# Kernel optimization log

Measured on AMD Instinct MI355X. Metric: run time of the kernel, lower is better.

The kernel has to match this reference:

```python
import jax, jax.numpy as jnp
import numpy as np

B, T, N, CIN, C, L, NC, S = 8, 64, 200, 200, 128, 2, 2, 100
SPARSITY = 30


def bn(x, g, b, eps=1e-5):
    # BatchNorm1d forward with batch statistics (training-mode math, biased var)
    m = x.mean(0)
    v = x.var(0)
    return (x - m) / jnp.sqrt(v + eps) * g + b


def ln(x, g, b, eps=1e-5):
    m = x.mean(-1, keepdims=True)
    v = x.var(-1, keepdims=True)
    return (x - m) / jnp.sqrt(v + eps) * g + b


def setup_inputs() -> dict:
    key = jax.random.key(0)
    ks = iter(jax.random.split(key, 64))

    def nrm(shape, s=0.02):
        return jax.random.normal(next(ks), shape, jnp.float32) * s

    return dict(
        fMRI_v=jax.random.normal(next(ks), (B, T, N, CIN), jnp.float32),
        fMRI_a=jax.random.uniform(next(ks), (B, T, N, N), jnp.float32),
        sMRI_trad=jax.random.normal(next(ks), (B, S), jnp.float32),
        sMRI_deep=jnp.zeros((B, 1, 8, 8, 8), jnp.float32),
        csatt=1, CA_MOD=0,
        w_init=nrm((CIN, C)), b_init=jnp.zeros((C,), jnp.float32),
        gin_eps=jnp.zeros((L,), jnp.float32),
        gin_w1=nrm((L, C, C)), gin_b1=jnp.zeros((L, C), jnp.float32),
        gin_bn1_g=jnp.ones((L, C), jnp.float32), gin_bn1_b=jnp.zeros((L, C), jnp.float32),
        gin_w2=nrm((L, C, C)), gin_b2=jnp.zeros((L, C), jnp.float32),
        gin_bn2_g=jnp.ones((L, C), jnp.float32), gin_bn2_b=jnp.zeros((L, C), jnp.float32),
        sero_w=nrm((L, C, C)), sero_b=jnp.zeros((L, C), jnp.float32),
        sero_bn_g=jnp.ones((L, C), jnp.float32), sero_bn_b=jnp.zeros((L, C), jnp.float32),
        sero_aw=nrm((L, C, N)), sero_ab=jnp.zeros((L, N), jnp.float32),
        tr_wqkv=nrm((L, C, 3 * C)), tr_bqkv=jnp.zeros((L, 3 * C), jnp.float32),
        tr_wo=nrm((L, C, C)), tr_bo=jnp.zeros((L, C), jnp.float32),
        tr_ln1_g=jnp.ones((L, C), jnp.float32), tr_ln1_b=jnp.zeros((L, C), jnp.float32),
        tr_ln2_g=jnp.ones((L, C), jnp.float32), tr_ln2_b=jnp.zeros((L, C), jnp.float32),
        tr_w1=nrm((L, C, 2 * C)), tr_b1=jnp.zeros((L, 2 * C), jnp.float32),
        tr_w2=nrm((L, 2 * C, C)), tr_b2=jnp.zeros((L, C), jnp.float32),
        cls_w=nrm((L, C, NC)), cls_b=jnp.zeros((L, NC), jnp.float32),
        smri_w=nrm((S, C)), smri_b=jnp.zeros((C,), jnp.float32),
        smri_bn_g=jnp.ones((C,), jnp.float32), smri_bn_b=jnp.zeros((C,), jnp.float32),
    )


def reference(fMRI_v, fMRI_a, sMRI_trad, sMRI_deep, csatt, CA_MOD,
              w_init, b_init, gin_eps,
              gin_w1, gin_b1, gin_bn1_g, gin_bn1_b,
              gin_w2, gin_b2, gin_bn2_g, gin_bn2_b,
              sero_w, sero_b, sero_bn_g, sero_bn_b, sero_aw, sero_ab,
              tr_wqkv, tr_bqkv, tr_wo, tr_bo,
              tr_ln1_g, tr_ln1_b, tr_ln2_g, tr_ln2_b,
              tr_w1, tr_b1, tr_w2, tr_b2,
              cls_w, cls_b, smri_w, smri_b, smri_bn_g, smri_bn_b):
    b, t, n = fMRI_a.shape[:3]
    # initial linear over flattened (b t n) tokens
    h3 = (fMRI_v.reshape(-1, fMRI_v.shape[-1]) @ w_init + b_init).reshape(b, t, n, -1)
    # _collate_adjacency: per-(sample,timepoint) percentile threshold -> block-diag sparse
    # with all-ones values; equivalent to a batched masked matmul.
    thr = jnp.percentile(fMRI_a, 100 - SPARSITY, axis=(-2, -1), keepdims=True)
    mask = (fMRI_a > thr).astype(h3.dtype)  # [b,t,n,n]

    logit = jnp.zeros((b, cls_w.shape[-1]), h3.dtype)
    latents, node_attns, time_attns = [], [], []
    scale = 1.0 / jnp.sqrt(jnp.asarray(h3.shape[-1], h3.dtype))
    for l in range(L):
        # LayerGIN: note the original feeds h3 (initial features) to EVERY layer
        agg = jnp.einsum('btij,btjc->btic', mask, h3) + gin_eps[l] * h3
        x = agg.reshape(-1, agg.shape[-1])
        x = jax.nn.relu(bn(x @ gin_w1[l] + gin_b1[l], gin_bn1_g[l], gin_bn1_b[l]))
        x = jax.nn.relu(bn(x @ gin_w2[l] + gin_b2[l], gin_bn2_g[l], gin_bn2_b[l]))
        hb = x.reshape(b, t, n, -1).transpose(1, 0, 2, 3)  # (t,b,n,c)
        # ModuleSERO readout (node_axis=2)
        xr = hb.mean(2)  # (t,b,c)
        e = jax.nn.gelu(bn(xr.reshape(t * b, -1) @ sero_w[l] + sero_b[l],
                           sero_bn_g[l], sero_bn_b[l]), approximate=False)
        ga = jax.nn.sigmoid(e @ sero_aw[l] + sero_ab[l]).reshape(t, b, n)
        hr = (hb * ga[..., None]).mean(2)  # (t,b,c)
        node_attns.append(ga.transpose(1, 0, 2))  # (b,t,n)
        # ModuleTransformer (single head, post-LN, no residual before ln1)
        qkv = hr @ tr_wqkv[l] + tr_bqkv[l]
        q, k, v = jnp.split(qkv, 3, axis=-1)
        A = jax.nn.softmax(jnp.einsum('tbc,sbc->bts', q, k) * scale, axis=-1)  # (b,t,t)
        att = jnp.einsum('bts,sbc->tbc', A, v) @ tr_wo[l] + tr_bo[l]
        x1 = ln(att, tr_ln1_g[l], tr_ln1_b[l])
        m = jax.nn.relu(x1 @ tr_w1[l] + tr_b1[l]) @ tr_w2[l] + tr_b2[l]
        x2 = ln(x1 + m, tr_ln2_g[l], tr_ln2_b[l])
        time_attns.append(A)
        lat = x2.sum(0)  # cls_token='sum' over time
        logit = logit + lat @ cls_w[l] + cls_b[l]
        latents.append(lat)
    feat_fMRI = jnp.stack(latents, 1).mean(1)  # (b,c)
    feat_sMRI = bn(sMRI_trad @ smri_w + smri_b, smri_bn_g, smri_bn_b)
    node_attn = jnp.stack(node_attns, 1)  # (b,L,t,n)
    time_attn = jnp.stack(time_attns, 1)  # (b,L,t,t)
    return (logit, feat_fMRI, feat_sMRI, node_attn, time_attn)
```

## Files before the change

### kernel.cpp

```cpp
#include <hip/hip_runtime.h>
#include <math.h>

#define B_   8
#define T_   64
#define N_   200
#define CIN_ 200
#define C_   128
#define L_   2
#define NC_  2
#define S_   100
#define BT_  512
#define RB_  102400

typedef __attribute__((ext_vector_type(8))) short short8v;
typedef __attribute__((ext_vector_type(4))) float f32x4v;

union U4S8 { uint4 u; short8v s; };

__device__ __forceinline__ unsigned short f2bf(float f) {
    unsigned u = __float_as_uint(f);
    unsigned r = (u + 0x7FFFu + ((u >> 16) & 1u)) >> 16;
    return (unsigned short)r;
}
__device__ __forceinline__ float bf2f(unsigned short u) {
// ... 85 lines not shown
        __syncthreads();
    }
    int c_lo_tot = red[0];
    if (tid < 256) part[tid] = hist[4*tid] + hist[4*tid+1] + hist[4*tid+2] + hist[4*tid+3];
    __syncthreads();
    if (tid < 32) {
        int s = 0;
        for (int i = 0; i < 8; i++) s += part[8*tid + i];
        grp[tid] = s;
    }
    __syncthreads();
    if (tid == 0) {
        int r = 27999 - c_lo_tot;
        int cum = 0, g = 0;
        while (cum + grp[g] <= r) cum += grp[g++];
        int t = g * 8;
        while (cum + part[t] <= r) cum += part[t++];
        int b = t * 4;
        while (cum + hist[b] <= r) cum += hist[b++];
        meta[2] = b; meta[3] = cum;
        int r1 = r + 1;
        cum = 0; g = 0;
        while (cum + grp[g] <= r1) cum += grp[g++];
        t = g * 8;
        while (cum + part[t] <= r1) cum += part[t++];
        b = t * 4;
        while (cum + hist[b] <= r1) cum += hist[b++];
        meta[4] = b; meta[5] = r;
    }
    __syncthreads();
    int blo = meta[2], base = meta[3], bhi = meta[4], r = meta[5];
    int m = meta[0]; if (m > 6144) m = 6144;
    for (int i = tid; i < m; i += 1024) {
        float v = candV[i];
        int bin = (int)((v - 0.65f) * 10240.0f);
        bin = bin < 0 ? 0 : (bin > 1023 ? 1023 : bin);
        if (bin >= blo && bin <= bhi) {
            int p = atomicAdd(&meta[1], 1);
            if (p < 256) cand2[p] = v;
        }
    }
    __syncthreads();
    if (tid == 0) {
        int m2 = meta[1]; if (m2 > 256) m2 = 256;
        for (int i = 1; i < m2; i++) {
            float key = cand2[i]; int j = i - 1;
            while (j >= 0 && cand2[j] > key) { cand2[j+1] = cand2[j]; j--; }
            cand2[j+1] = key;
        }
        float s1 = cand2[r - base], s2 = cand2[r + 1 - base];
        float tv = s1 * 0.701171875f + s2 * 0.298828125f;
        thr[bt] = tv;
        s_thr = tv;
    }
    __syncthreads();
    float tv = s_thr;
    for (int i = tid; i < m; i += 1024) {
        if (candV[i] > tv) {
            int vi = candP[i];
            int row = vi / 200, col = vi - row * 200;
            atomicOr(&smask[row * 7 + (col >> 5)], 1u << (col & 31));
        }
    }
    __syncthreads();
    for (int i = tid; i < 1400; i += 1024)
        msk[(long)bt * 1400 + i] = smask[i];
}

__global__ void wtcvt5_kernel(const float* __restrict__ w_init,
                              const float* __restrict__ gin_w1,
                              const float* __restrict__ gin_w2,
                              unsigned short* __restrict__ WT0,
                              unsigned short* __restrict__ WT1,
                              unsigned short* __restrict__ WT2) {
    int grp = blockIdx.x >> 7, c = blockIdx.x & 127;
    const float* w; unsigned short* wt; int K, Kpad;
    if (grp == 0)      { w = w_init;                     wt = WT0;                     K = 200; Kpad = 224; }
    else if (grp <= 2) { w = gin_w1 + (grp - 1) * C_ * C_; wt = WT1 + (grp - 1) * 128 * 128; K = 128; Kpad = 128; }
    else               { w = gin_w2 + (grp - 3) * C_ * C_; wt = WT2 + (grp - 3) * 128 * 128; K = 128; Kpad = 128; }
    for (int k = threadIdx.x; k < Kpad; k += 64)
        wt[(long)c * Kpad + k] = f2bf((k < K) ? w[(long)k * 128 + c] : 0.f);
}

template<bool A_BF16, bool BN_IN, bool BIAS_OUT, bool STATS_OUT>
__global__ __launch_bounds__(256) void gemm_direct_kernel(
        const void* __restrict__ xv, int K, int Kstride, int Ksteps,
        const unsigned short* __restrict__ wt, int Kpad,
        const float* __restrict__ bias, const float* __restrict__ statsIn,
        const float* __restrict__ bng, const float* __restrict__ bnb,
        unsigned short* __restrict__ y, float* __restrict__ statsOut) {
    constexpr int ASZ  = A_BF16 ? 8192 : 16384;
    constexpr int BOFF = 2 * ASZ;
    constexpr int NEED = 2 * ASZ + 2 * 8192;
    constexpr int POOL = NEED > 32768 ? NEED : 32768;
    __shared__ unsigned char pool[POOL];
    __shared__ float bnS[128], bnB[128];
    int tid = threadIdx.x;
    if (BN_IN) {
        if (tid < 128) {
            float mm = statsIn[tid] * (1.f / (float)RB_);
            float var = fmaxf(statsIn[128 + tid] * (1.f / (float)RB_) - mm * mm, 0.f);
            float sc = bng[tid] / sqrtf(var + 1e-5f);
            bnS[tid] = sc; bnB[tid] = bnb[tid] - mm * sc;
        }
    }
    int wave = tid >> 6, lane = tid & 63, quad = lane >> 4, m16 = lane & 15;
    long row0g = (long)blockIdx.x * 128;

    auto STAGE = [&](int buf, int ks) {
        #pragma unroll
        for (int j = 0; j < 2; j++) {
            int r = j * 64 + (tid >> 2);
            int c = (tid & 3) ^ ((r >> 1) & 3);
            const char* src = (const char*)wt + (long)r * (Kpad * 2) + ks * 64 + c * 16;
            char* dst = (char*)pool + BOFF + buf * 8192 + j * 4096 + wave * 1024;
            GLL(src, dst);
        }
        if (A_BF16) {
            const char* xb = (const char*)xv;
            #pragma unroll
            for (int j = 0; j < 2; j++) {
                int r = j * 64 + (tid >> 2);
                int c = (tid & 3) ^ ((r >> 1) & 3);
                const char* src = xb + ((row0g + r) * Kstride + ks * 32) * 2 + c * 16;
                char* dst = (char*)pool + buf * ASZ + j * 4096 + wave * 1024;
                GLL(src, dst);
            }
        } else {
            const char* xb = (const char*)xv;
            #pragma unroll
            for (int j = 0; j < 4; j++) {
                int r = j * 32 + (tid >> 3);
                int c = (tid & 7) ^ (r & 7);
                const char* src = xb + ((row0g + r) * Kstride + ks * 32) * 4 + c * 16;
                char* dst = (char*)pool + buf * ASZ + j * 4096 + wave * 1024;
                GLL(src, dst);
            }
        }
    };

    f32x4v acc[2][8];
    #pragma unroll
    for (int i = 0; i < 2; i++)
        #pragma unroll
        for (int j = 0; j < 8; j++) acc[i][j] = (f32x4v){0.f, 0.f, 0.f, 0.f};

    STAGE(0, 0);
    __syncthreads();

    for (int ks = 0; ks < Ksteps; ks++) {
        if (ks + 1 < Ksteps) {
            STAGE((ks + 1) & 1, ks + 1);
            if (A_BF16) asm volatile("s_waitcnt vmcnt(4)" ::: "memory");
            else        asm volatile("s_waitcnt vmcnt(6)" ::: "memory");
        } else {
            asm volatile("s_waitcnt vmcnt(0)" ::: "memory");
        }
        __builtin_amdgcn_s_barrier();
        asm volatile("" ::: "memory");

        const char* Ab = (const char*)pool + (ks & 1) * ASZ;
        const char* Bb = (const char*)pool + BOFF + (ks & 1) * 8192;
        int kf = ks * 32 + quad * 8;
        U4S8 bU[8];
        #pragma unroll
        for (int nt = 0; nt < 8; nt++) {
            int r = nt * 16 + m16;
            int ch = quad ^ ((r >> 1) & 3);
            bU[nt].u = *(const uint4*)(Bb + r * 64 + ch * 16);
        }
        U4S8 aU[2];
        if (A_BF16) {
            #pragma unroll
            for (int mt = 0; mt < 2; mt++) {
                int r = wave * 32 + mt * 16 + m16;
                int ch = quad ^ ((r >> 1) & 3);
                aU[mt].u = *(const uint4*)(Ab + r * 64 + ch * 16);
            }
            if (BN_IN) {
                float4 s0 = *(const float4*)&bnS[kf], s1 = *(const float4*)&bnS[kf + 4];
                float4 b0 = *(const float4*)&bnB[kf], b1 = *(const float4*)&bnB[kf + 4];
                #pragma unroll
                for (int mt = 0; mt < 2; mt++) {
                    uint4 u = aU[mt].u;
                    float f0 = fmaxf(bflo(u.x) * s0.x + b0.x, 0.f);
                    float f1 = fmaxf(bfhi(u.x) * s0.y + b0.y, 0.f);
                    float f2 = fmaxf(bflo(u.y) * s0.z + b0.z, 0.f);
                    float f3 = fmaxf(bfhi(u.y) * s0.w + b0.w, 0.f);
                    float f4 = fmaxf(bflo(u.z) * s1.x + b1.x, 0.f);
                    float f5 = fmaxf(bfhi(u.z) * s1.y + b1.y, 0.f);
                    float f6 = fmaxf(bflo(u.w) * s1.z + b1.z, 0.f);
                    float f7 = fmaxf(bfhi(u.w) * s1.w + b1.w, 0.f);
                    u.x = packbf(f0, f1); u.y = packbf(f2, f3);
                    u.z = packbf(f4, f5); u.w = packbf(f6, f7);
                    aU[mt].u = u;
                }
            }
        } else {
            #pragma unroll
            for (int mt = 0; mt < 2; mt++) {
                int r = wave * 32 + mt * 16 + m16;
                int swz = r & 7;
                const char* base = Ab + r * 128;
                float4 v0 = *(const float4*)(base + ((2 * quad) ^ swz) * 16);
                float4 v1 = *(const float4*)(base + ((2 * quad + 1) ^ swz) * 16);
                uint4 o;
                o.x = packbf(v0.x, v0.y); o.y = packbf(v0.z, v0.w);
                o.z = packbf(v1.x, v1.y); o.w = packbf(v1.z, v1.w);
                aU[mt].u = o;
            }
        }
        #pragma unroll
        for (int nt = 0; nt < 8; nt++) {
            acc[0][nt] = __builtin_amdgcn_mfma_f32_16x16x32_bf16(aU[0].s, bU[nt].s, acc[0][nt], 0, 0, 0);
            acc[1][nt] = __builtin_amdgcn_mfma_f32_16x16x32_bf16(aU[1].s, bU[nt].s, acc[1][nt], 0, 0, 0);
        }
        asm volatile("s_waitcnt lgkmcnt(0)" ::: "memory");
        __builtin_amdgcn_s_barrier();
        asm volatile("" ::: "memory");
    }
    if (!A_BF16 && (K & 31) != 0) {
        int kf = Ksteps * 32 + quad * 8;
        U4S8 bU[8];
        #pragma unroll
        for (int nt = 0; nt < 8; nt++)
            bU[nt].u = *(const uint4*)&wt[(long)(nt * 16 + m16) * Kpad + kf];
        U4S8 aU[2];
        const float* x = (const float*)xv;
        #pragma unroll
        for (int mt = 0; mt < 2; mt++) {
            uint4 o = {0u, 0u, 0u, 0u};
            if (kf + 8 <= K) {
                const float* p = &x[(row0g + wave * 32 + mt * 16 + m16) * Kstride + kf];
                float4 v0 = *(const float4*)p;
                float4 v1 = *(const float4*)(p + 4);
                o.x = packbf(v0.x, v0.y); o.y = packbf(v0.z, v0.w);
                o.z = packbf(v1.x, v1.y); o.w = packbf(v1.z, v1.w);
            }
            aU[mt].u = o;
        }
        #pragma unroll
        for (int nt = 0; nt < 8; nt++) {
            acc[0][nt] = __builtin_amdgcn_mfma_f32_16x16x32_bf16(aU[0].s, bU[nt].s, acc[0][nt], 0, 0, 0);
            acc[1][nt] = __builtin_amdgcn_mfma_f32_16x16x32_bf16(aU[1].s, bU[nt].s, acc[1][nt], 0, 0, 0);
        }
    }

    unsigned short* trans = (unsigned short*)pool;
    float sAcc[8], qAcc[8];
    #pragma unroll
    for (int nt = 0; nt < 8; nt++) {
        int col = nt * 16 + m16;
        float bv = BIAS_OUT ? bias[col] : 0.f;
        float s = 0.f, q = 0.f;
        #pragma unroll
        for (int mt = 0; mt < 2; mt++) {
            int lrb = wave * 32 + mt * 16 + quad * 4;
            #pragma unroll
            for (int i = 0; i < 4; i++) {
                int lr = lrb + i;
                float v = acc[mt][nt][i] + bv;
                trans[lr * 128 + (col ^ ((lr & 6) << 2))] = f2bf(v);
                if (STATS_OUT) { s += v; q += v * v; }
            }
        }
        sAcc[nt] = s; qAcc[nt] = q;
    }
    __syncthreads();
    #pragma unroll
    for (int rnd = 0; rnd < 8; rnd++) {
        int row = rnd * 16 + (tid >> 4), ch = tid & 15;
        uint4 v = *(const uint4*)&trans[row * 128 + ((ch * 8) ^ ((row & 6) << 2))];
        *(uint4*)&y[(row0g + row) * 128 + ch * 8] = v;
    }
    if (STATS_OUT) {
        __syncthreads();
        float* redS = (float*)pool;
        float* redQ = redS + 2048;
        #pragma unroll
        for (int nt = 0; nt < 8; nt++) {
            int col = nt * 16 + m16;
            redS[col * 16 + wave * 4 + quad] = sAcc[nt];
            redQ[col * 16 + wave * 4 + quad] = qAcc[nt];
        }
        __syncthreads();
        if (tid < 128) {
            float s = 0.f, q = 0.f;
            #pragma unroll
            for (int j = 0; j < 16; j++) { s += redS[tid * 16 + j]; q += redQ[tid * 16 + j]; }
            atomicAdd(&statsOut[tid], s);
            atomicAdd(&statsOut[128 + tid], q);
        }
    }
}

__global__ __launch_bounds__(256) void h3gemmT_kernel(
        const float* __restrict__ xv, const unsigned short* __restrict__ wt,
        const float* __restrict__ bias,
        unsigned short* __restrict__ yrow, unsigned short* __restrict__ zt) {
    __shared__ unsigned char pool[49152];
    int tid = threadIdx.x;
    int wave = tid >> 6, lane = tid & 63, quad = lane >> 4, m16 = lane & 15;
    long row0g = (long)blockIdx.x * 128;

    auto STAGE = [&](int buf, int ks) {
        #pragma unroll
        for (int j = 0; j < 2; j++) {
            int r = j * 64 + (tid >> 2);
            int c = (tid & 3) ^ ((r >> 1) & 3);
            const char* src = (const char*)wt + (long)r * 448 + ks * 64 + c * 16;
            char* dst = (char*)pool + 32768 + buf * 8192 + j * 4096 + wave * 1024;
            GLL(src, dst);
        }
        const char* xb = (const char*)xv;
        #pragma unroll
        for (int j = 0; j < 4; j++) {
            int r = j * 32 + (tid >> 3);
            int c = (tid & 7) ^ (r & 7);
            const char* src = xb + ((row0g + r) * 200 + ks * 32) * 4 + c * 16;
            char* dst = (char*)pool + buf * 16384 + j * 4096 + wave * 1024;
            GLL(src, dst);
        }
    };

    f32x4v acc[2][8];
    #pragma unroll
    for (int i = 0; i < 2; i++)
        #pragma unroll
        for (int j = 0; j < 8; j++) acc[i][j] = (f32x4v){0.f, 0.f, 0.f, 0.f};

    STAGE(0, 0);
    __syncthreads();

    for (int ks = 0; ks < 6; ks++) {
        if (ks + 1 < 6) {
            STAGE((ks + 1) & 1, ks + 1);
            asm volatile("s_waitcnt vmcnt(6)" ::: "memory");
        } else {
            asm volatile("s_waitcnt vmcnt(0)" ::: "memory");
        }
        __builtin_amdgcn_s_barrier();
        asm volatile("" ::: "memory");

        const char* Ab = (const char*)pool + (ks & 1) * 16384;
        const char* Bb = (const char*)pool + 32768 + (ks & 1) * 8192;
        U4S8 bU[8];
        #pragma unroll
        for (int nt = 0; nt < 8; nt++) {
            int r = nt * 16 + m16;
            int ch = quad ^ ((r >> 1) & 3);
            bU[nt].u = *(const uint4*)(Bb + r * 64 + ch * 16);
        }
        U4S8 aU[2];
        #pragma unroll
        for (int mt = 0; mt < 2; mt++) {
            int r = wave * 32 + mt * 16 + m16;
            int swz = r & 7;
            const char* base = Ab + r * 128;
            float4 v0 = *(const float4*)(base + ((2 * quad) ^ swz) * 16);
            float4 v1 = *(const float4*)(base + ((2 * quad + 1) ^ swz) * 16);
            uint4 o;
            o.x = packbf(v0.x, v0.y); o.y = packbf(v0.z, v0.w);
            o.z = packbf(v1.x, v1.y); o.w = packbf(v1.z, v1.w);
            aU[mt].u = o;
        }
        #pragma unroll
        for (int nt = 0; nt < 8; nt++) {
            acc[0][nt] = __builtin_amdgcn_mfma_f32_16x16x32_bf16(aU[0].s, bU[nt].s, acc[0][nt], 0, 0, 0);
            acc[1][nt] = __builtin_amdgcn_mfma_f32_16x16x32_bf16(aU[1].s, bU[nt].s, acc[1][nt], 0, 0, 0);
        }
        asm volatile("s_waitcnt lgkmcnt(0)" ::: "memory");
        __builtin_amdgcn_s_barrier();
        asm volatile("" ::: "memory");
    }
    {
        int kf = 192 + quad * 8;
        U4S8 bU[8];
        #pragma unroll
        for (int nt = 0; nt < 8; nt++)
            bU[nt].u = *(const uint4*)&wt[(long)(nt * 16 + m16) * 224 + kf];
        U4S8 aU[2];
        #pragma unroll
        for (int mt = 0; mt < 2; mt++) {
            uint4 o = {0u, 0u, 0u, 0u};
            if (kf + 8 <= 200) {
                const float* p = &xv[(row0g + wave * 32 + mt * 16 + m16) * 200 + kf];
                float4 v0 = *(const float4*)p;
                float4 v1 = *(const float4*)(p + 4);
                o.x = packbf(v0.x, v0.y); o.y = packbf(v0.z, v0.w);
                o.z = packbf(v1.x, v1.y); o.w = packbf(v1.z, v1.w);
            }
            aU[mt].u = o;
        }
        #pragma unroll
        for (int nt = 0; nt < 8; nt++) {
            acc[0][nt] = __builtin_amdgcn_mfma_f32_16x16x32_bf16(aU[0].s, bU[nt].s, acc[0][nt], 0, 0, 0);
            acc[1][nt] = __builtin_amdgcn_mfma_f32_16x16x32_bf16(aU[1].s, bU[nt].s, acc[1][nt], 0, 0, 0);
        }
    }

    unsigned short* tile = (unsigned short*)pool;
    #pragma unroll
    for (int nt = 0; nt < 8; nt++) {
        int col = nt * 16 + m16;
        float bv = bias[col];
        #pragma unroll
        for (int mt = 0; mt < 2; mt++) {
            int lrb = wave * 32 + mt * 16 + quad * 4;
            #pragma unroll
            for (int i = 0; i < 4; i++) {
                int lr = lrb + i;
                tile[lr * 128 + (col ^ ((lr & 14) << 2))] = f2bf(acc[mt][nt][i] + bv);
            }
        }
    }
    __syncthreads();
    #pragma unroll
    for (int rnd = 0; rnd < 8; rnd++) {
        int row = rnd * 16 + (tid >> 4), ch = tid & 15;
        uint4 v = *(const uint4*)&tile[row * 128 + ((ch * 8) ^ ((row & 14) << 2))];
        *(uint4*)&yrow[(row0g + row) * 128 + ch * 8] = v;
    }
    int r0 = blockIdx.x * 128;
    int bt0 = r0 / 200, n0 = r0 - bt0 * 200;
    int len0 = 200 - n0; if (len0 > 128) len0 = 128;
    int c = tid & 127, h = tid >> 7;
    #pragma unroll
    for (int u = 0; u < 8; u++) {
        int rl = h * 64 + u * 8;
        unsigned short e[8];
        #pragma unroll
        for (int j = 0; j < 8; j++)
            e[j] = tile[(rl + j) * 128 + (c ^ (((rl + j) & 14) << 2))];
        uint4 o;
        o.x = (unsigned)e[0] | ((unsigned)e[1] << 16);
        o.y = (unsigned)e[2] | ((unsigned)e[3] << 16);
        o.z = (unsigned)e[4] | ((unsigned)e[5] << 16);
        o.w = (unsigned)e[6] | ((unsigned)e[7] << 16);
        int bt, n;
        if (rl < len0) { bt = bt0; n = n0 + rl; } else { bt = bt0 + 1; n = rl - len0; }
        *(uint4*)&zt[((long)bt * 128 + c) * 224 + n] = o;
    }
    if (n0 >= 72) {
        uint4 z = {0u, 0u, 0u, 0u};
        for (int idx = tid; idx < 384; idx += 256) {
            int c2 = idx & 127, u2 = idx >> 7;
            *(uint4*)&zt[((long)bt0 * 128 + c2) * 224 + 200 + u2 * 8] = z;
        }
    }
}

__global__ __launch_bounds__(256) void maskfused_kernel(
        const unsigned* __restrict__ msk, const unsigned short* __restrict__ zt,
        const unsigned short* __restrict__ h3, const unsigned short* __restrict__ w1t,
        const float* __restrict__ geps, int l, const float* __restrict__ b1,
        unsigned short* __restrict__ y, float* __restrict__ statsOut) {
    __shared__ union {
        unsigned short stage[4][4096];
        unsigned short trans[16384];
        struct { float S[2048]; float Q[2048]; } red;
    } u;
    __shared__ unsigned sbits[128 * 7];
    int tid = threadIdx.x;
    int bt = blockIdx.x & 511, half = blockIdx.x >> 9;
    int row0 = half * 128;
    int wave = tid >> 6, lane = tid & 63, quad = lane >> 4, m16 = lane & 15;
    const char* ztb = (const char*)(zt + (long)bt * 128 * 224);

    int sr = tid >> 2, sq = tid & 3;
    auto STAGE = [&](int buf, int kc) {
        #pragma unroll
        for (int j = 0; j < 2; j++) {
            int r = j * 64 + sr;
            int q = sq ^ ((r >> 1) & 3);
            const char* src = ztb + r * 448 + kc * 64 + q * 16;
            char* dst = (char*)&u.stage[buf][0] + j * 4096 + wave * 1024;
            GLL(src, dst);
        }
    };

    STAGE(0, 0); STAGE(1, 1); STAGE(2, 2);
    for (int idx = tid; idx < 896; idx += 256) {
        int gr = row0 + idx / 7;
        sbits[idx] = (gr < N_) ? msk[(long)bt * 1400 + gr * 7 + (idx % 7)] : 0u;
    }
    unsigned ONEu = 0x3F80u;

    f32x4v acc[2][8];
    #pragma unroll
    for (int i = 0; i < 2; i++)
        #pragma unroll
        for (int j = 0; j < 8; j++) acc[i][j] = (f32x4v){0.f, 0.f, 0.f, 0.f};

    __syncthreads();

    for (int kc = 0; kc < 7; kc++) {
        if (kc < 4) STAGE((kc + 3) & 3, kc + 3);
        if (kc == 3)      asm volatile("s_waitcnt vmcnt(6)" ::: "memory");
        else if (kc == 4) asm volatile("s_waitcnt vmcnt(4)" ::: "memory");
        else if (kc == 5) asm volatile("s_waitcnt vmcnt(2)" ::: "memory");
        else if (kc == 6) asm volatile("s_waitcnt vmcnt(0)" ::: "memory");
        __builtin_amdgcn_s_barrier();
        asm volatile("" ::: "memory");

        const char* sb = (const char*)&u.stage[kc & 3][0];
        U4S8 bU[8];
        #pragma unroll
        for (int nt = 0; nt < 8; nt++) {
            int r = nt * 16 + m16;
            int q = quad ^ ((r >> 1) & 3);
            bU[nt].u = *(const uint4*)(sb + r * 64 + q * 16);
        }
        U4S8 aU[2];
        #pragma unroll
        for (int mt = 0; mt < 2; mt++) {
            int lr = wave * 32 + mt * 16 + m16;
            unsigned bits = (sbits[lr * 7 + kc] >> (quad * 8)) & 0xFFu;
            unsigned o[4];
            #pragma unroll
            for (int p = 0; p < 4; p++) {
                unsigned lo = ((bits >> (2 * p)) & 1u) ? ONEu : 0u;
                unsigned hi = ((bits >> (2 * p + 1)) & 1u) ? ONEu : 0u;
                o[p] = lo | (hi << 16);
            }
            aU[mt].u = make_uint4(o[0], o[1], o[2], o[3]);
        }
        #pragma unroll
        for (int nt = 0; nt < 8; nt++) {
            acc[0][nt] = __builtin_amdgcn_mfma_f32_16x16x32_bf16(aU[0].s, bU[nt].s, acc[0][nt], 0, 0, 0);
            acc[1][nt] = __builtin_amdgcn_mfma_f32_16x16x32_bf16(aU[1].s, bU[nt].s, acc[1][nt], 0, 0, 0);
        }
        asm volatile("s_waitcnt lgkmcnt(0)" ::: "memory");
        __builtin_amdgcn_s_barrier();
        asm volatile("" ::: "memory");
    }

    #pragma unroll
    for (int nt = 0; nt < 8; nt++) {
        int col = nt * 16 + m16;
        #pragma unroll
        for (int mt = 0; mt < 2; mt++) {
            int lrb = wave * 32 + mt * 16 + quad * 4;
            #pragma unroll
            for (int i = 0; i < 4; i++) {
                int lr = lrb + i;
                u.trans[lr * 128 + (col ^ ((lr & 6) << 2))] = f2bf(acc[mt][nt][i]);
            }
        }
    }
    __syncthreads();

    float eps = geps[l];
    f32x4v acc2[2][8];
    #pragma unroll
    for (int i = 0; i < 2; i++)
        #pragma unroll
        for (int j = 0; j < 8; j++) acc2[i][j] = (f32x4v){0.f, 0.f, 0.f, 0.f};

    for (int ks = 0; ks < 4; ks++) {
        int kf = ks * 32 + quad * 8;
        U4S8 bU[8];
        #pragma unroll
        for (int nt = 0; nt < 8; nt++)
            bU[nt].u = *(const uint4*)&w1t[(long)(nt * 16 + m16) * 128 + kf];
        U4S8 aU[2];
        #pragma unroll
        for (int mt = 0; mt < 2; mt++) {
            int r = wave * 32 + mt * 16 + m16;
            uint4 mu = *(const uint4*)&u.trans[r * 128 + (kf ^ ((r & 6) << 2))];
            int gr = row0 + r;
            uint4 hu = {0u, 0u, 0u, 0u};
            if (gr < N_) hu = *(const uint4*)&h3[((long)bt * N_ + gr) * 128 + kf];
            float f0 = bflo(mu.x) + eps * bflo(hu.x);
            float f1 = bfhi(mu.x) + eps * bfhi(hu.x);
            float f2 = bflo(mu.y) + eps * bflo(hu.y);
            float f3 = bfhi(mu.y) + eps * bfhi(hu.y);
            float f4 = bflo(mu.z) + eps * bflo(hu.z);
            float f5 = bfhi(mu.z) + eps * bfhi(hu.z);
            float f6 = bflo(mu.w) + eps * bflo(hu.w);
            float f7 = bfhi(mu.w) + eps * bfhi(hu.w);
            uint4 o;
            o.x = packbf(f0, f1); o.y = packbf(f2, f3);
            o.z = packbf(f4, f5); o.w = packbf(f6, f7);
            aU[mt].u = o;
        }
        #pragma unroll
        for (int nt = 0; nt < 8; nt++) {
            acc2[0][nt] = __builtin_amdgcn_mfma_f32_16x16x32_bf16(aU[0].s, bU[nt].s, acc2[0][nt], 0, 0, 0);
            acc2[1][nt] = __builtin_amdgcn_mfma_f32_16x16x32_bf16(aU[1].s, bU[nt].s, acc2[1][nt], 0, 0, 0);
        }
    }
    __syncthreads();

    float sAcc[8], qAcc[8];
    #pragma unroll
    for (int nt = 0; nt < 8; nt++) {
        int col = nt * 16 + m16;
        float bv = b1[col];
        float s = 0.f, q = 0.f;
        #pragma unroll
        for (int mt = 0; mt < 2; mt++) {
            int lrb = wave * 32 + mt * 16 + quad * 4;
            #pragma unroll
            for (int i = 0; i < 4; i++) {
                int lr = lrb + i;
                float v = acc2[mt][nt][i] + bv;
                u.trans[lr * 128 + (col ^ ((lr & 6) << 2))] = f2bf(v);
                if (row0 + lr < N_) { s += v; q += v * v; }
            }
        }
        sAcc[nt] = s; qAcc[nt] = q;
    }
    __syncthreads();
    #pragma unroll
    for (int rnd = 0; rnd < 8; rnd++) {
        int row = rnd * 16 + (tid >> 4), ch = tid & 15;
        int gr = row0 + row;
        uint4 v = *(const uint4*)&u.trans[row * 128 + ((ch * 8) ^ ((row & 6) << 2))];
        if (gr < N_)
            *(uint4*)&y[((long)bt * N_ + gr) * 128 + ch * 8] = v;
    }
    __syncthreads();
    #pragma unroll
    for (int nt = 0; nt < 8; nt++) {
        int col = nt * 16 + m16;
        u.red.S[col * 16 + wave * 4 + quad] = sAcc[nt];
        u.red.Q[col * 16 + wave * 4 + quad] = qAcc[nt];
    }
    __syncthreads();
    if (tid < 128) {
        float s = 0.f, q = 0.f;
        #pragma unroll
        for (int j = 0; j < 16; j++) { s += u.red.S[tid * 16 + j]; q += u.red.Q[tid * 16 + j]; }
        atomicAdd(&statsOut[tid], s);
        atomicAdd(&statsOut[128 + tid], q);
    }
}

__global__ __launch_bounds__(256) void xrE_kernel(
        const unsigned short* __restrict__ raw, const float* __restrict__ stats,
        const float* __restrict__ g, const float* __restrict__ b,
        const float* __restrict__ sw, const float* __restrict__ sb,
        float* __restrict__ E, float* __restrict__ statE) {
    __shared__ float red[256];
    __shared__ float xrrow[128];
    int tid = threadIdx.x, c = tid & 127, hf = tid >> 7;
    int t = blockIdx.x / B_, bb = blockIdx.x % B_;
    const unsigned short* base = raw + ((long)bb * T_ + t) * N_ * C_;
    float m = stats[c] * (1.f / (float)RB_);
    float var = fmaxf(stats[128 + c] * (1.f / (float)RB_) - m * m, 0.f);
    float sc = g[c] / sqrtf(var + 1e-5f);
    float sh = b[c] - m * sc;
    float s = 0.f;
    for (int n = hf * 100; n < hf * 100 + 100; n++)
        s += fmaxf(fmaf(bf2f(base[n * C_ + c]), sc, sh), 0.f);
    red[tid] = s;
    __syncthreads();
    if (hf == 0) xrrow[c] = (red[c] + red[c + 128]) * (1.f / 200.f);
    __syncthreads();
    float acc = 0.f;
    for (int k = hf * 64; k < hf * 64 + 64; k++)
        acc = fmaf(xrrow[k], sw[k * C_ + c], acc);
    red[tid] = acc;
    __syncthreads();
    if (hf == 0) {
        float v = red[c] + red[c + 128] + sb[c];
        E[(long)blockIdx.x * C_ + c] = v;
        atomicAdd(&statE[c], v);
        atomicAdd(&statE[C_ + c], v * v);
    }
}

__global__ __launch_bounds__(256) void ga_kernel(const float* __restrict__ eRaw,
                          const float* __restrict__ stats,
                          const float* __restrict__ sg, const float* __restrict__ sb,
                          const float* __restrict__ aw, const float* __restrict__ ab,
                          float* __restrict__ ga, float* __restrict__ node_out, int l) {
    __shared__ float sx[4 * C_];
    __shared__ float bnS[C_], bnB[C_];
    int tid = threadIdx.x;
    if (tid < C_) {
        float m = stats[tid] * (1.f / (float)BT_);
        float var = fmaxf(stats[C_ + tid] * (1.f / (float)BT_) - m * m, 0.f);
        float inv = 1.f / sqrtf(var + 1e-5f);
        float sc = inv * sg[tid];
        bnS[tid] = sc;
        bnB[tid] = sb[tid] - m * sc;
    }
    __syncthreads();
    long r0 = (long)blockIdx.x * 4;
    for (int idx = tid; idx < 4 * C_; idx += 256) {
        int col = idx & (C_ - 1);
        float v = eRaw[r0 * C_ + idx] * bnS[col] + bnB[col];
        sx[idx] = 0.5f * v * (1.f + erff(v * 0.70710678118654752f));
    }
    __syncthreads();
    int c = tid;
    if (c < N_) {
        float acc[4] = {0.f, 0.f, 0.f, 0.f};
        for (int k = 0; k < C_; k++) {
            float wv = aw[k * N_ + c];
            #pragma unroll
            for (int i = 0; i < 4; i++) acc[i] = fmaf(sx[i * C_ + k], wv, acc[i]);
        }
        float bv = ab[c];
        for (int i = 0; i < 4; i++) {
            int tb = (int)r0 + i;
            int t = tb / B_, b = tb % B_;
            float v = 1.f / (1.f + expf(-(acc[i] + bv)));
            ga[(long)tb * N_ + c] = v;
            node_out[(((long)b * L_ + l) * T_ + t) * N_ + c] = v;
        }
    }
}

__global__ __launch_bounds__(256) void hrQKV_kernel(
// ... 165 lines not shown
    float inv = 1.f / sqrtf(var + 1e-5f);
    for (int b = 0; b < B_; b++) out[b * C_ + c] = (y[b] - m) * inv * g[c] + bb[c];
}

extern "C" void kernel_launch(void* const* d_in, const int* in_sizes, int n_in,
                              void* d_out, int out_size, void* d_ws, size_t ws_size,
                              hipStream_t stream) {
    const float* fv       = (const float*)d_in[0];
    const float* fa       = (const float*)d_in[1];
    const float* trad     = (const float*)d_in[2];
    const float* w_init   = (const float*)d_in[6];
    const float* b_init   = (const float*)d_in[7];
    const float* gin_eps  = (const float*)d_in[8];
    const float* gin_w1   = (const float*)d_in[9];
    const float* gin_b1   = (const float*)d_in[10];
    const float* gbn1g    = (const float*)d_in[11];
    const float* gbn1b    = (const float*)d_in[12];
    const float* gin_w2   = (const float*)d_in[13];
    const float* gin_b2   = (const float*)d_in[14];
    const float* gbn2g    = (const float*)d_in[15];
    const float* gbn2b    = (const float*)d_in[16];
    const float* sero_w   = (const float*)d_in[17];
    const float* sero_b   = (const float*)d_in[18];
    const float* sbng     = (const float*)d_in[19];
    const float* sbnb     = (const float*)d_in[20];
    const float* sero_aw  = (const float*)d_in[21];
    const float* sero_ab  = (const float*)d_in[22];
    const float* wqkv     = (const float*)d_in[23];
    const float* bqkv     = (const float*)d_in[24];
    const float* wo       = (const float*)d_in[25];
    const float* bo       = (const float*)d_in[26];
    const float* ln1g     = (const float*)d_in[27];
    const float* ln1b     = (const float*)d_in[28];
    const float* ln2g     = (const float*)d_in[29];
    const float* ln2b     = (const float*)d_in[30];
    const float* tw1      = (const float*)d_in[31];
    const float* tb1      = (const float*)d_in[32];
    const float* tw2      = (const float*)d_in[33];
    const float* tb2      = (const float*)d_in[34];
    const float* cls_w    = (const float*)d_in[35];
    const float* cls_b    = (const float*)d_in[36];
    const float* smri_w   = (const float*)d_in[37];
    const float* smri_b   = (const float*)d_in[38];
    const float* smri_g   = (const float*)d_in[39];
    const float* smri_bb  = (const float*)d_in[40];

    float* out = (float*)d_out;

    const long SZ_BIG = (long)RB_ * C_;
    unsigned short* H3b = (unsigned short*)d_ws;
    unsigned short* Y1b = H3b + SZ_BIG;
    unsigned short* Y2b = Y1b + SZ_BIG;
    unsigned short* ZTb = Y2b + SZ_BIG;
    float* fbase = (float*)(ZTb + (long)BT_ * 128 * 224);
    float* THR  = fbase;
    float* SBUF = THR + 512;
    float* LAT  = SBUF + 1536;
    float* E    = LAT + 2048;
    float* GA   = E + BT_ * C_;
    float* QKV  = GA + BT_ * N_;
    float* X1   = QKV + BT_ * 3 * C_;
    unsigned short* WT0 = (unsigned short*)(X1 + BT_ * C_);
    unsigned short* WT1 = WT0 + 128 * 224;
    unsigned short* WT2 = WT1 + 2 * 128 * 128;
    unsigned* MSK = (unsigned*)(WT2 + 2 * 128 * 128);

    float* OUT_LOGIT = out;
    float* OUT_FEATS = out + 1040;
    float* OUT_NODE  = out + 2064;
    float* OUT_TIME  = out + 206864;

    wtcvt5_kernel<<<640, 64, 0, stream>>>(w_init, gin_w1, gin_w2, WT0, WT1, WT2);
    hipMemsetAsync(SBUF, 0, (1536 + 2048) * sizeof(float), stream);

    h3gemmT_kernel<<<RB_ / 128, 256, 0, stream>>>(fv, WT0, b_init, H3b, ZTb);
    thr_kernel<<<BT_, 1024, 0, stream>>>(fa, THR, MSK);

    for (int l = 0; l < L_; l++) {
        float* SA = SBUF + l * 768;
        float* SB = SA + 256;
        float* SE = SA + 512;
        maskfused_kernel<<<BT_ * 2, 256, 0, stream>>>(MSK, ZTb, H3b, WT1 + l * 128 * 128,
            gin_eps, l, gin_b1 + l * C_, Y2b, SA);
        gemm_direct_kernel<true, true, true, true><<<RB_ / 128, 256, 0, stream>>>(
            Y2b, 128, 128, 4, WT2 + l * 128 * 128, 128, gin_b2 + l * C_, SA,
            gbn1g + l * C_, gbn1b + l * C_, Y1b, SB);
        xrE_kernel<<<BT_, 256, 0, stream>>>(Y1b, SB, gbn2g + l * C_, gbn2b + l * C_,
            sero_w + l * C_ * C_, sero_b + l * C_, E, SE);
        ga_kernel<<<BT_ / 4, 256, 0, stream>>>(E, SE, sbng + l * C_, sbnb + l * C_,
            sero_aw + l * C_ * N_, sero_ab + l * N_, GA, OUT_NODE, l);
        hrQKV_kernel<<<BT_, 256, 0, stream>>>(Y1b, SB, gbn2g + l * C_, gbn2b + l * C_,
            GA, wqkv + l * C_ * 3 * C_, bqkv + l * 3 * C_, QKV);
        attnln_kernel<<<BT_, 128, 0, stream>>>(QKV, wo + l * C_ * C_, bo + l * C_,
            ln1g + l * C_, ln1b + l * C_, OUT_TIME, X1, l);
        ffn_kernel<<<BT_ / 2, 256, 0, stream>>>(X1, tw1 + l * C_ * 2 * C_, tb1 + l * 2 * C_,
            tw2 + l * 2 * C_ * C_, tb2 + l * C_, ln2g + l * C_, ln2b + l * C_,
            LAT + l * B_ * C_);
    }

    final_kernel<<<5, 256, 0, stream>>>(LAT, cls_w, cls_b, OUT_LOGIT);
    smri_kernel<<<1, 128, 0, stream>>>(trad, smri_w, smri_b, smri_g, smri_bb, OUT_FEATS);
}
```

Baseline: 713.4 us.

## Preload full K tiles into 64KB LDS, replacing double-buffered staging in GEMM kernels

The templated gemm_direct kernel becomes a specialized bngemm kernel that issues all four K-step loads for A and B into a 64KB LDS pool up front. One barrier follows, then the K loop runs with no per-step waits or barriers. maskfused_kernel likewise loads all seven K-chunks at once instead of using a 4-deep rotating stage, and keeps separate LDS regions for the aggregate and transpose buffers so one barrier can be dropped. This removes per-iteration vmcnt waits and barriers, but 64KB+ of LDS per block cuts occupancy to about one or two blocks per CU, which reduces latency hiding across blocks.

```diff
diff --git a/kernel.cpp b/kernel.cpp
--- a/kernel.cpp
+++ b/kernel.cpp
@@ -191,85 +191,55 @@
         wt[(long)c * Kpad + k] = f2bf((k < K) ? w[(long)k * 128 + c] : 0.f);
 }
 
-template<bool A_BF16, bool BN_IN, bool BIAS_OUT, bool STATS_OUT>
-__global__ __launch_bounds__(256) void gemm_direct_kernel(
-        const void* __restrict__ xv, int K, int Kstride, int Ksteps,
-        const unsigned short* __restrict__ wt, int Kpad,
+__global__ __launch_bounds__(256) void bngemm_kernel(
+        const unsigned short* __restrict__ xb,
+        const unsigned short* __restrict__ wt,
         const float* __restrict__ bias, const float* __restrict__ statsIn,
         const float* __restrict__ bng, const float* __restrict__ bnb,
         unsigned short* __restrict__ y, float* __restrict__ statsOut) {
-    constexpr int ASZ  = A_BF16 ? 8192 : 16384;
-    constexpr int BOFF = 2 * ASZ;
-    constexpr int NEED = 2 * ASZ + 2 * 8192;
-    constexpr int POOL = NEED > 32768 ? NEED : 32768;
-    __shared__ unsigned char pool[POOL];
+    __shared__ unsigned char pool[65536];
     __shared__ float bnS[128], bnB[128];
     int tid = threadIdx.x;
-    if (BN_IN) {
-        if (tid < 128) {
-            float mm = statsIn[tid] * (1.f / (float)RB_);
-            float var = fmaxf(statsIn[128 + tid] * (1.f / (float)RB_) - mm * mm, 0.f);
-            float sc = bng[tid] / sqrtf(var + 1e-5f);
-            bnS[tid] = sc; bnB[tid] = bnb[tid] - mm * sc;
-        }
-    }
     int wave = tid >> 6, lane = tid & 63, quad = lane >> 4, m16 = lane & 15;
     long row0g = (long)blockIdx.x * 128;
 
-    auto STAGE = [&](int buf, int ks) {
-        #pragma unroll
-        for (int j = 0; j < 2; j++) {
-            int r = j * 64 + (tid >> 2);
-            int c = (tid & 3) ^ ((r >> 1) & 3);
-            const char* src = (const char*)wt + (long)r * (Kpad * 2) + ks * 64 + c * 16;
-            char* dst = (char*)pool + BOFF + buf * 8192 + j * 4096 + wave * 1024;
-            GLL(src, dst);
-        }
-        if (A_BF16) {
-            const char* xb = (const char*)xv;
-            #pragma unroll
-            for (int j = 0; j < 2; j++) {
-                int r = j * 64 + (tid >> 2);
-                int c = (tid & 3) ^ ((r >> 1) & 3);
-                const char* src = xb + ((row0g + r) * Kstride + ks * 32) * 2 + c * 16;
-                char* dst = (char*)pool + buf * ASZ + j * 4096 + wave * 1024;
-                GLL(src, dst);
-            }
-        } else {
-            const char* xb = (const char*)xv;
-            #pragma unroll
-            for (int j = 0; j < 4; j++) {
-                int r = j * 32 + (tid >> 3);
-                int c = (tid & 7) ^ (r & 7);
-                const char* src = xb + ((row0g + r) * Kstride + ks * 32) * 4 + c * 16;
-                char* dst = (char*)pool + buf * ASZ + j * 4096 + wave * 1024;
-                GLL(src, dst);
-            }
-        }
-    };
-
+    {
+        int r0 = tid >> 2;
+        int csw = (tid & 3) ^ ((r0 >> 1) & 3);
+        int r1 = 64 + (tid >> 2);
+        int csw1 = (tid & 3) ^ ((r1 >> 1) & 3);
+        #pragma unroll
+        for (int ks = 0; ks < 4; ks++) {
+            char* Adst = (char*)pool + ks * 16384;
+            char* Bdst = Adst + 8192;
+            GLL((const char*)xb + ((row0g + r0) * 128 + ks * 32) * 2 + csw * 16,
+                Adst + wave * 1024);
+            GLL((const char*)xb + ((row0g + r1) * 128 + ks * 32) * 2 + csw1 * 16,
+                Adst + 4096 + wave * 1024);
+            GLL((const char*)wt + (long)r0 * 256 + ks * 64 + csw * 16,
+                Bdst + wave * 1024);
+            GLL((const char*)wt + (long)r1 * 256 + ks * 64 + csw1 * 16,
+                Bdst + 4096 + wave * 1024);
+        }
+    }
+    if (tid < 128) {
+        float mm = statsIn[tid] * (1.f / (float)RB_);
+        float var = fmaxf(statsIn[128 + tid] * (1.f / (float)RB_) - mm * mm, 0.f);
+        float sc = bng[tid] / sqrtf(var + 1e-5f);
+        bnS[tid] = sc; bnB[tid] = bnb[tid] - mm * sc;
+    }
     f32x4v acc[2][8];
     #pragma unroll
     for (int i = 0; i < 2; i++)
         #pragma unroll
         for (int j = 0; j < 8; j++) acc[i][j] = (f32x4v){0.f, 0.f, 0.f, 0.f};
 
-    STAGE(0, 0);
-    __syncthreads();
-
-    for (int ks = 0; ks < Ksteps; ks++) {
-        if (ks + 1 < Ksteps) {
-            STAGE((ks + 1) & 1, ks + 1);
-            if (A_BF16) asm volatile("s_waitcnt vmcnt(4)" ::: "memory");
-            else        asm volatile("s_waitcnt vmcnt(6)" ::: "memory");
-        } else {
-            asm volatile("s_waitcnt vmcnt(0)" ::: "memory");
-        }
-        __builtin_amdgcn_s_barrier();
-        asm volatile("" ::: "memory");
-
-        const char* Ab = (const char*)pool + (ks & 1) * ASZ;
-        const char* Bb = (const char*)pool + BOFF + (ks & 1) * 8192;
+    __syncthreads();
+
+    #pragma unroll 1
+    for (int ks = 0; ks < 4; ks++) {
+        const char* Ab = (const char*)pool + ks * 16384;
+        const char* Bb = Ab + 8192;
         int kf = ks * 32 + quad * 8;
         U4S8 bU[8];
         #pragma unroll
@@ -279,88 +249,43 @@
             bU[nt].u = *(const uint4*)(Bb + r * 64 + ch * 16);
         }
         U4S8 aU[2];
-        if (A_BF16) {
-            #pragma unroll
-            for (int mt = 0; mt < 2; mt++) {
-                int r = wave * 32 + mt * 16 + m16;
-                int ch = quad ^ ((r >> 1) & 3);
-                aU[mt].u = *(const uint4*)(Ab + r * 64 + ch * 16);
-            }
-            if (BN_IN) {
-                float4 s0 = *(const float4*)&bnS[kf], s1 = *(const float4*)&bnS[kf + 4];
-                float4 b0 = *(const float4*)&bnB[kf], b1 = *(const float4*)&bnB[kf + 4];
-                #pragma unroll
-                for (int mt = 0; mt < 2; mt++) {
-                    uint4 u = aU[mt].u;
-                    float f0 = fmaxf(bflo(u.x) * s0.x + b0.x, 0.f);
-                    float f1 = fmaxf(bfhi(u.x) * s0.y + b0.y, 0.f);
-                    float f2 = fmaxf(bflo(u.y) * s0.z + b0.z, 0.f);
-                    float f3 = fmaxf(bfhi(u.y) * s0.w + b0.w, 0.f);
-                    float f4 = fmaxf(bflo(u.z) * s1.x + b1.x, 0.f);
-                    float f5 = fmaxf(bfhi(u.z) * s1.y + b1.y, 0.f);
-                    float f6 = fmaxf(bflo(u.w) * s1.z + b1.z, 0.f);
-                    float f7 = fmaxf(bfhi(u.w) * s1.w + b1.w, 0.f);
-                    u.x = packbf(f0, f1); u.y = packbf(f2, f3);
-                    u.z = packbf(f4, f5); u.w = packbf(f6, f7);
-                    aU[mt].u = u;
-                }
-            }
-        } else {
-            #pragma unroll
-            for (int mt = 0; mt < 2; mt++) {
-                int r = wave * 32 + mt * 16 + m16;
-                int swz = r & 7;
-                const char* base = Ab + r * 128;
-                float4 v0 = *(const float4*)(base + ((2 * quad) ^ swz) * 16);
-                float4 v1 = *(const float4*)(base + ((2 * quad + 1) ^ swz) * 16);
-                uint4 o;
-                o.x = packbf(v0.x, v0.y); o.y = packbf(v0.z, v0.w);
-                o.z = packbf(v1.x, v1.y); o.w = packbf(v1.z, v1.w);
-                aU[mt].u = o;
-            }
+        #pragma unroll
+        for (int mt = 0; mt < 2; mt++) {
+            int r = wave * 32 + mt * 16 + m16;
+            int ch = quad ^ ((r >> 1) & 3);
+            aU[mt].u = *(const uint4*)(Ab + r * 64 + ch * 16);
+        }
+        float4 s0 = *(const float4*)&bnS[kf], s1 = *(const float4*)&bnS[kf + 4];
+        float4 b0 = *(const float4*)&bnB[kf], b1 = *(const float4*)&bnB[kf + 4];
+        #pragma unroll
+        for (int mt = 0; mt < 2; mt++) {
+            uint4 u = aU[mt].u;
+            float f0 = fmaxf(bflo(u.x) * s0.x + b0.x, 0.f);
+            float f1 = fmaxf(bfhi(u.x) * s0.y + b0.y, 0.f);
+            float f2 = fmaxf(bflo(u.y) * s0.z + b0.z, 0.f);
+            float f3 = fmaxf(bfhi(u.y) * s0.w + b0.w, 0.f);
+            float f4 = fmaxf(bflo(u.z) * s1.x + b1.x, 0.f);
+            float f5 = fmaxf(bfhi(u.z) * s1.y + b1.y, 0.f);
+            float f6 = fmaxf(bflo(u.w) * s1.z + b1.z, 0.f);
+            float f7 = fmaxf(bfhi(u.w) * s1.w + b1.w, 0.f);
+            u.x = packbf(f0, f1); u.y = packbf(f2, f3);
+            u.z = packbf(f4, f5); u.w = packbf(f6, f7);
+            aU[mt].u = u;
         }
         #pragma unroll
         for (int nt = 0; nt < 8; nt++) {
             acc[0][nt] = __builtin_amdgcn_mfma_f32_16x16x32_bf16(aU[0].s, bU[nt].s, acc[0][nt], 0, 0, 0);
             acc[1][nt] = __builtin_amdgcn_mfma_f32_16x16x32_bf16(aU[1].s, bU[nt].s, acc[1][nt], 0, 0, 0);
         }
-        asm volatile("s_waitcnt lgkmcnt(0)" ::: "memory");
-        __builtin_amdgcn_s_barrier();
-        asm volatile("" ::: "memory");
-    }
-    if (!A_BF16 && (K & 31) != 0) {
-        int kf = Ksteps * 32 + quad * 8;
-        U4S8 bU[8];
-        #pragma unroll
-        for (int nt = 0; nt < 8; nt++)
-            bU[nt].u = *(const uint4*)&wt[(long)(nt * 16 + m16) * Kpad + kf];
-        U4S8 aU[2];
-        const float* x = (const float*)xv;
-        #pragma unroll
-        for (int mt = 0; mt < 2; mt++) {
-            uint4 o = {0u, 0u, 0u, 0u};
-            if (kf + 8 <= K) {
-                const float* p = &x[(row0g + wave * 32 + mt * 16 + m16) * Kstride + kf];
-                float4 v0 = *(const float4*)p;
-                float4 v1 = *(const float4*)(p + 4);
-                o.x = packbf(v0.x, v0.y); o.y = packbf(v0.z, v0.w);
-                o.z = packbf(v1.x, v1.y); o.w = packbf(v1.z, v1.w);
-            }
-            aU[mt].u = o;
-        }
-        #pragma unroll
-        for (int nt = 0; nt < 8; nt++) {
-            acc[0][nt] = __builtin_amdgcn_mfma_f32_16x16x32_bf16(aU[0].s, bU[nt].s, acc[0][nt], 0, 0, 0);
-            acc[1][nt] = __builtin_amdgcn_mfma_f32_16x16x32_bf16(aU[1].s, bU[nt].s, acc[1][nt], 0, 0, 0);
-        }
-    }
-
+    }
+
+    __syncthreads();
     unsigned short* trans = (unsigned short*)pool;
     float sAcc[8], qAcc[8];
     #pragma unroll
     for (int nt = 0; nt < 8; nt++) {
         int col = nt * 16 + m16;
-        float bv = BIAS_OUT ? bias[col] : 0.f;
+        float bv = bias[col];
         float s = 0.f, q = 0.f;
         #pragma unroll
         for (int mt = 0; mt < 2; mt++) {
@@ -370,7 +295,7 @@
                 int lr = lrb + i;
                 float v = acc[mt][nt][i] + bv;
                 trans[lr * 128 + (col ^ ((lr & 6) << 2))] = f2bf(v);
-                if (STATS_OUT) { s += v; q += v * v; }
+                s += v; q += v * v;
             }
         }
         sAcc[nt] = s; qAcc[nt] = q;
@@ -382,24 +307,22 @@
         uint4 v = *(const uint4*)&trans[row * 128 + ((ch * 8) ^ ((row & 6) << 2))];
         *(uint4*)&y[(row0g + row) * 128 + ch * 8] = v;
     }
-    if (STATS_OUT) {
-        __syncthreads();
-        float* redS = (float*)pool;
-        float* redQ = redS + 2048;
-        #pragma unroll
-        for (int nt = 0; nt < 8; nt++) {
-            int col = nt * 16 + m16;
-            redS[col * 16 + wave * 4 + quad] = sAcc[nt];
-            redQ[col * 16 + wave * 4 + quad] = qAcc[nt];
-        }
-        __syncthreads();
-        if (tid < 128) {
-            float s = 0.f, q = 0.f;
-            #pragma unroll
-            for (int j = 0; j < 16; j++) { s += redS[tid * 16 + j]; q += redQ[tid * 16 + j]; }
-            atomicAdd(&statsOut[tid], s);
-            atomicAdd(&statsOut[128 + tid], q);
-        }
+    __syncthreads();
+    float* redS = (float*)pool;
+    float* redQ = redS + 2048;
+    #pragma unroll
+    for (int nt = 0; nt < 8; nt++) {
+        int col = nt * 16 + m16;
+        redS[col * 16 + wave * 4 + quad] = sAcc[nt];
+        redQ[col * 16 + wave * 4 + quad] = qAcc[nt];
+    }
+    __syncthreads();
+    if (tid < 128) {
+        float s = 0.f, q = 0.f;
+        #pragma unroll
+        for (int j = 0; j < 16; j++) { s += redS[tid * 16 + j]; q += redQ[tid * 16 + j]; }
+        atomicAdd(&statsOut[tid], s);
+        atomicAdd(&statsOut[128 + tid], q);
     }
 }
 
@@ -564,11 +487,7 @@
         const unsigned short* __restrict__ h3, const unsigned short* __restrict__ w1t,
         const float* __restrict__ geps, int l, const float* __restrict__ b1,
         unsigned short* __restrict__ y, float* __restrict__ statsOut) {
-    __shared__ union {
-        unsigned short stage[4][4096];
-        unsigned short trans[16384];
-        struct { float S[2048]; float Q[2048]; } red;
-    } u;
+    __shared__ unsigned char pool[65536];
     __shared__ unsigned sbits[128 * 7];
     int tid = threadIdx.x;
     int bt = blockIdx.x & 511, half = blockIdx.x >> 9;
@@ -576,19 +495,18 @@
     int wave = tid >> 6, lane = tid & 63, quad = lane >> 4, m16 = lane & 15;
     const char* ztb = (const char*)(zt + (long)bt * 128 * 224);
 
-    int sr = tid >> 2, sq = tid & 3;
-    auto STAGE = [&](int buf, int kc) {
-        #pragma unroll
-        for (int j = 0; j < 2; j++) {
-            int r = j * 64 + sr;
-            int q = sq ^ ((r >> 1) & 3);
-            const char* src = ztb + r * 448 + kc * 64 + q * 16;
-            char* dst = (char*)&u.stage[buf][0] + j * 4096 + wave * 1024;
-            GLL(src, dst);
-        }
-    };
-
-    STAGE(0, 0); STAGE(1, 1); STAGE(2, 2);
+    {
+        int r0 = tid >> 2;
+        int q0 = (tid & 3) ^ ((r0 >> 1) & 3);
+        int r1 = 64 + (tid >> 2);
+        int q1 = (tid & 3) ^ ((r1 >> 1) & 3);
+        #pragma unroll
+        for (int kc = 0; kc < 7; kc++) {
+            char* dst = (char*)pool + kc * 8192;
+            GLL(ztb + r0 * 448 + kc * 64 + q0 * 16, dst + wave * 1024);
+            GLL(ztb + r1 * 448 + kc * 64 + q1 * 16, dst + 4096 + wave * 1024);
+        }
+    }
     for (int idx = tid; idx < 896; idx += 256) {
         int gr = row0 + idx / 7;
         sbits[idx] = (gr < N_) ? msk[(long)bt * 1400 + gr * 7 + (idx % 7)] : 0u;
@@ -603,16 +521,9 @@
 
     __syncthreads();
 
+    #pragma unroll 1
     for (int kc = 0; kc < 7; kc++) {
-        if (kc < 4) STAGE((kc + 3) & 3, kc + 3);
-        if (kc == 3)      asm volatile("s_waitcnt vmcnt(6)" ::: "memory");
-        else if (kc == 4) asm volatile("s_waitcnt vmcnt(4)" ::: "memory");
-        else if (kc == 5) asm volatile("s_waitcnt vmcnt(2)" ::: "memory");
-        else if (kc == 6) asm volatile("s_waitcnt vmcnt(0)" ::: "memory");
-        __builtin_amdgcn_s_barrier();
-        asm volatile("" ::: "memory");
-
-        const char* sb = (const char*)&u.stage[kc & 3][0];
+        const char* sb = (const char*)pool + kc * 8192;
         U4S8 bU[8];
         #pragma unroll
         for (int nt = 0; nt < 8; nt++) {
@@ -639,11 +550,11 @@
             acc[0][nt] = __builtin_amdgcn_mfma_f32_16x16x32_bf16(aU[0].s, bU[nt].s, acc[0][nt], 0, 0, 0);
             acc[1][nt] = __builtin_amdgcn_mfma_f32_16x16x32_bf16(aU[1].s, bU[nt].s, acc[1][nt], 0, 0, 0);
         }
-        asm volatile("s_waitcnt lgkmcnt(0)" ::: "memory");
-        __builtin_amdgcn_s_barrier();
-        asm volatile("" ::: "memory");
-    }
-
+    }
+    __syncthreads();
+
+    unsigned short* magg = (unsigned short*)pool;
+    unsigned short* trans = (unsigned short*)(pool + 32768);
     #pragma unroll
     for (int nt = 0; nt < 8; nt++) {
         int col = nt * 16 + m16;
@@ -653,7 +564,7 @@
             #pragma unroll
             for (int i = 0; i < 4; i++) {
                 int lr = lrb + i;
-                u.trans[lr * 128 + (col ^ ((lr & 6) << 2))] = f2bf(acc[mt][nt][i]);
+                magg[lr * 128 + (col ^ ((lr & 6) << 2))] = f2bf(acc[mt][nt][i]);
             }
         }
     }
@@ -666,6 +577,7 @@
         #pragma unroll
         for (int j = 0; j < 8; j++) acc2[i][j] = (f32x4v){0.f, 0.f, 0.f, 0.f};
 
+    #pragma unroll 1
     for (int ks = 0; ks < 4; ks++) {
         int kf = ks * 32 + quad * 8;
         U4S8 bU[8];
@@ -676,7 +588,7 @@
         #pragma unroll
         for (int mt = 0; mt < 2; mt++) {
             int r = wave * 32 + mt * 16 + m16;
-            uint4 mu = *(const uint4*)&u.trans[r * 128 + (kf ^ ((r & 6) << 2))];
+            uint4 mu = *(const uint4*)&magg[r * 128 + (kf ^ ((r & 6) << 2))];
             int gr = row0 + r;
             uint4 hu = {0u, 0u, 0u, 0u};
             if (gr < N_) hu = *(const uint4*)&h3[((long)bt * N_ + gr) * 128 + kf];
@@ -699,7 +611,6 @@
             acc2[1][nt] = __builtin_amdgcn_mfma_f32_16x16x32_bf16(aU[1].s, bU[nt].s, acc2[1][nt], 0, 0, 0);
         }
     }
-    __syncthreads();
 
     float sAcc[8], qAcc[8];
     #pragma unroll
@@ -714,7 +625,7 @@
             for (int i = 0; i < 4; i++) {
                 int lr = lrb + i;
                 float v = acc2[mt][nt][i] + bv;
-                u.trans[lr * 128 + (col ^ ((lr & 6) << 2))] = f2bf(v);
+                trans[lr * 128 + (col ^ ((lr & 6) << 2))] = f2bf(v);
                 if (row0 + lr < N_) { s += v; q += v * v; }
             }
         }
@@ -725,22 +636,24 @@
     for (int rnd = 0; rnd < 8; rnd++) {
         int row = rnd * 16 + (tid >> 4), ch = tid & 15;
         int gr = row0 + row;
-        uint4 v = *(const uint4*)&u.trans[row * 128 + ((ch * 8) ^ ((row & 6) << 2))];
+        uint4 v = *(const uint4*)&trans[row * 128 + ((ch * 8) ^ ((row & 6) << 2))];
         if (gr < N_)
             *(uint4*)&y[((long)bt * N_ + gr) * 128 + ch * 8] = v;
     }
     __syncthreads();
+    float* redS = (float*)(pool + 32768);
+    float* redQ = redS + 2048;
     #pragma unroll
     for (int nt = 0; nt < 8; nt++) {
         int col = nt * 16 + m16;
-        u.red.S[col * 16 + wave * 4 + quad] = sAcc[nt];
-        u.red.Q[col * 16 + wave * 4 + quad] = qAcc[nt];
+        redS[col * 16 + wave * 4 + quad] = sAcc[nt];
+        redQ[col * 16 + wave * 4 + quad] = qAcc[nt];
     }
     __syncthreads();
     if (tid < 128) {
         float s = 0.f, q = 0.f;
         #pragma unroll
-        for (int j = 0; j < 16; j++) { s += u.red.S[tid * 16 + j]; q += u.red.Q[tid * 16 + j]; }
+        for (int j = 0; j < 16; j++) { s += redS[tid * 16 + j]; q += redQ[tid * 16 + j]; }
         atomicAdd(&statsOut[tid], s);
         atomicAdd(&statsOut[128 + tid], q);
     }
@@ -1072,8 +985,8 @@
         float* SE = SA + 512;
         maskfused_kernel<<<BT_ * 2, 256, 0, stream>>>(MSK, ZTb, H3b, WT1 + l * 128 * 128,
             gin_eps, l, gin_b1 + l * C_, Y2b, SA);
-        gemm_direct_kernel<true, true, true, true><<<RB_ / 128, 256, 0, stream>>>(
-            Y2b, 128, 128, 4, WT2 + l * 128 * 128, 128, gin_b2 + l * C_, SA,
+        bngemm_kernel<<<RB_ / 128, 256, 0, stream>>>(
+            Y2b, WT2 + l * 128 * 128, gin_b2 + l * C_, SA,
             gbn1g + l * C_, gbn1b + l * C_, Y1b, SB);
         xrE_kernel<<<BT_, 256, 0, stream>>>(Y1b, SB, gbn2g + l * C_, gbn2b + l * C_,
             sero_w + l * C_ * C_, sero_b + l * C_, E, SE);
```

Result: no change. 706.0 us (-1.0%).
